# Kernel tuning notes

Hardware: AMD Instinct MI355X
Metric: run time of the kernel (lower is better)

Reference implementation:

```python
import jax, jax.numpy as jnp
import numpy as np

D_MODEL = 2048
D_STATE = 64
D_CONV = 4
EXPAND = 2
HEADDIM = 64
NGROUPS = 1
CHUNK = 64
D_INNER = EXPAND * D_MODEL            # 4096
NHEADS = D_INNER // HEADDIM           # 64
D_XBC = D_INNER + 2 * NGROUPS * D_STATE
D_IN_PROJ = 2 * D_INNER + 2 * NGROUPS * D_STATE + NHEADS


def setup_inputs():
    key = jax.random.key(0)
    ks = jax.random.split(key, 8)
    B, L = 2, 4096
    u = jax.random.normal(ks[0], (B, L, D_MODEL), jnp.float32)
    W_in = jax.random.normal(ks[1], (D_IN_PROJ, D_MODEL), jnp.float32) * 0.02
    conv_w = jax.random.normal(ks[2], (D_XBC, D_CONV), jnp.float32) * 0.2
    conv_b = jnp.zeros((D_XBC,), jnp.float32)
    dt = jnp.exp(jax.random.uniform(ks[3], (NHEADS,)) * (np.log(0.1) - np.log(0.001)) + np.log(0.001))
    dt = jnp.clip(dt, 1e-4)
    dt_bias = dt + jnp.log(-jnp.expm1(-dt))
    A_log = jnp.log(jax.random.uniform(ks[4], (NHEADS,), minval=1.0, maxval=16.0))
    D_param = jnp.ones((NHEADS,), jnp.float32)
    norm_w = jnp.ones((D_INNER,), jnp.float32)
    W_out = jax.random.normal(ks[5], (D_MODEL, D_INNER), jnp.float32) * 0.02
    return dict(u=u, W_in=W_in, conv_w=conv_w, conv_b=conv_b, dt_bias=dt_bias,
                A_log=A_log, D_param=D_param, norm_w=norm_w, W_out=W_out)


def segsum(x):
    # x: (..., T) -> (..., T, T) with entry [l,s] = sum_{s< i <= l} x[i], -inf above diag
    T = x.shape[-1]
    mask_strict = jnp.tril(jnp.ones((T, T), bool), k=-1)
    mask_incl = jnp.tril(jnp.ones((T, T), bool), k=0)
    xe = jnp.where(mask_strict, x[..., :, None], 0.0)  # element [l,s] = x[l] if l>s
    xseg = jnp.cumsum(xe, axis=-2)
    return jnp.where(mask_incl, xseg, -jnp.inf)


def ssd_scan(X, A, Bm, Cm, block_len=CHUNK):
    # X: (b,L,h,p), A: (b,L,h), Bm/Cm: (b,L,h,n)
    b, seqlen, h, p = X.shape
    n = Bm.shape[-1]
    pad_len = (block_len - seqlen % block_len) % block_len
    if pad_len > 0:
        X = jnp.pad(X, ((0, 0), (0, pad_len), (0, 0), (0, 0)))
        A = jnp.pad(A, ((0, 0), (0, pad_len), (0, 0)))
        Bm = jnp.pad(Bm, ((0, 0), (0, pad_len), (0, 0), (0, 0)))
        Cm = jnp.pad(Cm, ((0, 0), (0, pad_len), (0, 0), (0, 0)))
    L = X.shape[1]
    c = L // block_len
    Xc = X.reshape(b, c, block_len, h, p)
    Ac = A.reshape(b, c, block_len, h).transpose(0, 3, 1, 2)  # (b,h,c,l)
    Bc = Bm.reshape(b, c, block_len, h, n)
    Cc = Cm.reshape(b, c, block_len, h, n)
    A_cum = jnp.cumsum(Ac, axis=-1)                           # (b,h,c,l)
    Lmat = jnp.exp(segsum(Ac))                                # (b,h,c,l,s)
    CB = jnp.einsum('bclhn,bcshn->bhcls', Cc, Bc)
    Y_diag = jnp.einsum('bhcls,bcshp->bhclp', CB * Lmat, Xc)
    decay_states = jnp.exp(A_cum[..., -1:] - A_cum)           # (b,h,c,l)
    states = jnp.einsum('bhcl,bclhn,bclhp->bhcpn', decay_states, Bc, Xc)
    init = jnp.zeros((b, h, 1, p, n), X.dtype)
    states = jnp.concatenate([init, states], axis=2)          # (b,h,c+1,p,n)
    chunk_decay = jnp.pad(A_cum[..., -1], ((0, 0), (0, 0), (1, 0)))  # (b,h,c+1)
    decay_chunk = jnp.exp(segsum(chunk_decay))                # (b,h,c+1,c+1)
    new_states = jnp.einsum('bhzc,bhcpn->bhzpn', decay_chunk, states)[:, :, :-1]
    Y_off = jnp.einsum('bclhn,bhcpn,bhcl->bhclp', Cc, new_states, jnp.exp(A_cum))
    Y = (Y_diag + Y_off).transpose(0, 2, 3, 1, 4).reshape(b, L, h, p)
    if pad_len > 0:
        Y = Y[:, :seqlen]
    return Y


def rmsnorm_grouped(x, w, ngroups, eps=1e-5):
    gs = x.shape[-1] // ngroups
    xg = x.reshape(*x.shape[:-1], ngroups, gs)
    xg = xg * jax.lax.rsqrt(jnp.mean(xg * xg, axis=-1, keepdims=True) + eps)
    return xg.reshape(x.shape) * w


def reference(u, W_in, conv_w, conv_b, dt_bias, A_log, D_param, norm_w, W_out):
    B, L, _ = u.shape
    zxbcdt = u @ W_in.T                                      # (B,L,d_in_proj)
    z = zxbcdt[..., :D_INNER]
    xBC = zxbcdt[..., D_INNER:D_INNER + D_XBC]
    dt = zxbcdt[..., D_INNER + D_XBC:]
    # causal depthwise conv1d, kernel D_CONV, left-pad D_CONV-1
    xpad = jnp.pad(xBC, ((0, 0), (D_CONV - 1, 0), (0, 0)))
    conv = conv_b
    for k in range(D_CONV):
        conv = conv + conv_w[:, k] * xpad[:, k:k + L, :]
    xBC = jax.nn.silu(conv)
    x = xBC[..., :D_INNER].reshape(B, L, NHEADS, HEADDIM)
    B_ssm = xBC[..., D_INNER:D_INNER + NGROUPS * D_STATE].reshape(B, L, NGROUPS, D_STATE)
    C_ssm = xBC[..., D_INNER + NGROUPS * D_STATE:].reshape(B, L, NGROUPS, D_STATE)
    if NGROUPS < NHEADS:
        rep = NHEADS // NGROUPS
        B_ssm = jnp.repeat(B_ssm, rep, axis=2)
        C_ssm = jnp.repeat(C_ssm, rep, axis=2)
    dt = jax.nn.softplus(dt + dt_bias)                        # (B,L,nheads)
    A = -jnp.exp(A_log)                                       # (nheads,)
    y = ssd_scan(x * dt[..., None], A * dt, B_ssm, C_ssm, block_len=CHUNK)
    y = y + D_param[:, None] * x
    y = y.reshape(B, L, D_INNER)
    y = rmsnorm_grouped(y * jax.nn.silu(z), norm_w, NGROUPS)
    return y @ W_out.T
```

## Files before the change

### kernel.cpp

```cpp
#include <hip/hip_runtime.h>
#include <hip/hip_bf16.h>
#include <math.h>

#define SEQ       4096
#define DMODEL    2048
#define DINNER    4096
#define DXBC      4224
#define NPROJ     8384
#define NHEADS    64
#define HDIM      64
#define DSTATE    64
#define NCHUNK    64
#define XLD       4352

typedef __attribute__((ext_vector_type(8))) _Float16 half8;
typedef __attribute__((ext_vector_type(2))) _Float16 half2v;
typedef __attribute__((ext_vector_type(4))) float floatx4;

__device__ __forceinline__ void async_copy16(void* lds, const void* g) {
  __builtin_amdgcn_global_load_lds(
      (const __attribute__((address_space(1))) unsigned int*)g,
      (__attribute__((address_space(3))) unsigned int*)lds, 16, 0, 0);
}

__device__ __forceinline__ float silu_f(float x) { return x / (1.f + __expf(-x)); }

__device__ __forceinline__ void cvt8(const float* __restrict__ s, _Float16* __restrict__ d) {
  float4 a = *(const float4*)s;
  float4 b = *(const float4*)(s + 4);
  half8 h;
  h[0] = (_Float16)a.x; h[1] = (_Float16)a.y; h[2] = (_Float16)a.z; h[3] = (_Float16)a.w;
  h[4] = (_Float16)b.x; h[5] = (_Float16)b.y; h[6] = (_Float16)b.z; h[7] = (_Float16)b.w;
  *(half8*)d = h;
}

__global__ void diag_kernel(float* out, float v) { out[0] = v; }

__global__ void cvt8_kernel(const float* __restrict__ src, _Float16* __restrict__ dst, int n8) {
  int i = blockIdx.x * 256 + threadIdx.x;
  if (i < n8) cvt8(src + (size_t)i * 8, dst + (size_t)i * 8);
}

#define U_N8 (SEQ * DMODEL / 8)
__global__ void cvt_in_kernel(const float* __restrict__ u, const float* __restrict__ W_in,
                              _Float16* __restrict__ ubf, _Float16* __restrict__ winbf) {
  int i = blockIdx.x * 256 + threadIdx.x;
  if (i < U_N8) {
    cvt8(u + (size_t)i * 8, ubf + (size_t)i * 8);
  } else {
    int j = i - U_N8;
    int row = j >> 8;
    size_t off = (size_t)j * 8;
    if (row < NPROJ) {
      cvt8(W_in + off, winbf + off);
    } else {
      half8 zz = {};
      *(half8*)(winbf + off) = zz;
    }
  }
}

template <typename OT>
__global__ __launch_bounds__(256) void gemm_bt64(
    const _Float16* __restrict__ A, const _Float16* __restrict__ B,
    OT* __restrict__ C0, OT* __restrict__ C1, int K,
    int ldc0, int ldc1, int ncol0, int tiles_m, int tiles_n) {
  __shared__ __align__(16) _Float16 As[128 * 64];
  __shared__ __align__(16) _Float16 Bs[128 * 64];
  int t = threadIdx.x;
  int nt = tiles_m * tiles_n;
  int id = blockIdx.x;
  int id2 = ((nt & 7) == 0) ? ((id & 7) * (nt >> 3) + (id >> 3)) : id;
  int wband = tiles_m << 2;
  int g = id2 / wband;
  int rm = id2 - g * wband;
  int bw = tiles_n - (g << 2); if (bw > 4) bw = 4;
  int pn = (g << 2) + rm % bw;
  int pm = rm / bw;
  int m0 = pm * 128, n0 = pn * 128;

  int w = t >> 6, lane = t & 63, q = lane >> 4, r = lane & 15;
  int wm = (w >> 1) * 64, wn = (w & 1) * 64;
  int rowoff = lane >> 3;
  int chunkoff = ((lane & 7) ^ rowoff) * 8;
  const _Float16* gA[4];
  const _Float16* gB[4];
#pragma unroll
  for (int i = 0; i < 4; ++i) {
    gA[i] = A + (size_t)(m0 + i * 32 + w * 8 + rowoff) * K + chunkoff;
    gB[i] = B + (size_t)(n0 + i * 32 + w * 8 + rowoff) * K + chunkoff;
  }
  floatx4 acc[4][4] = {};
  for (int k0 = 0; k0 < K; k0 += 64) {
#pragma unroll
    for (int i = 0; i < 4; ++i) {
      async_copy16(As + (i * 32 + w * 8) * 64, gA[i] + k0);
      async_copy16(Bs + (i * 32 + w * 8) * 64, gB[i] + k0);
    }
    __syncthreads();
#pragma unroll
    for (int kk = 0; kk < 64; kk += 32) {
      half8 af[4], bf[4];
#pragma unroll
      for (int im = 0; im < 4; ++im) {
        int R = wm + im * 16 + r;
        af[im] = *(const half8*)&As[R * 64 + ((((kk >> 3) + q) ^ (R & 7)) << 3)];
      }
#pragma unroll
      for (int in = 0; in < 4; ++in) {
        int R = wn + in * 16 + r;
        bf[in] = *(const half8*)&Bs[R * 64 + ((((kk >> 3) + q) ^ (R & 7)) << 3)];
      }
#pragma unroll
      for (int im = 0; im < 4; ++im)
#pragma unroll
        for (int in = 0; in < 4; ++in)
          acc[im][in] =
              __builtin_amdgcn_mfma_f32_16x16x32_f16(af[im], bf[in], acc[im][in], 0, 0, 0);
    }
    __syncthreads();
  }
  OT* Cp = (n0 < ncol0) ? C0 : C1;
  int ldc = (n0 < ncol0) ? ldc0 : ldc1;
  int cb = (n0 < ncol0) ? n0 : n0 - ncol0;
#pragma unroll
  for (int im = 0; im < 4; ++im)
#pragma unroll
    for (int in = 0; in < 4; ++in)
#pragma unroll
      for (int i = 0; i < 4; ++i)
        Cp[(size_t)(m0 + wm + im * 16 + q * 4 + i) * ldc + cb + wn + in * 16 + r] =
            (OT)acc[im][in][i];
}

template <typename OT>
__global__ __launch_bounds__(512, 2) void gemm256(
    const _Float16* __restrict__ A, const _Float16* __restrict__ B,
    OT* __restrict__ C0, OT* __restrict__ C1, int K,
    int ldc0, int ldc1, int ncol0, int tiles_m, int tiles_n) {
  __shared__ __align__(16) _Float16 As[2][256 * 64];
  __shared__ __align__(16) _Float16 Bs[2][256 * 64];
  int t = threadIdx.x;
  int nwg = tiles_m * tiles_n;
  int id = blockIdx.x;
  int wgid = ((nwg & 7) == 0) ? ((id & 7) * (nwg >> 3) + (id >> 3)) : id;
  int wband = tiles_m << 2;
  int g = wgid / wband;
  int rm = wgid - g * wband;
  int bw = tiles_n - (g << 2); if (bw > 4) bw = 4;
  int pn = (g << 2) + rm % bw;
  int pm = rm / bw;
  int m0 = pm * 256, n0 = pn * 256;

  int w = t >> 6, lane = t & 63, q4 = lane >> 4, r16 = lane & 15;
  int srow = lane >> 3;
  int schunk = ((lane & 7) ^ srow) << 3;
  const _Float16* gAb = A + (size_t)(m0 + w * 8 + srow) * K + schunk;
  const _Float16* gBb = B + (size_t)(n0 + w * 8 + srow) * K + schunk;
  int Ra = (w >> 2) * 128 + r16;
  int Rb = (w & 3) * 64 + r16;

  unsigned aLds = (unsigned)(unsigned long long)
      (const __attribute__((address_space(3))) void*)(const void*)&As[0][0];
  unsigned bLds = (unsigned)(unsigned long long)
      (const __attribute__((address_space(3))) void*)(const void*)&Bs[0][0];
  int x0 = (q4 ^ (r16 & 7)) << 4;
  int x1 = ((4 + q4) ^ (r16 & 7)) << 4;
  unsigned baseA00 = aLds + Ra * 128 + x0;
  unsigned baseA01 = aLds + Ra * 128 + x1;
  unsigned baseA10 = baseA00 + 32768;
  unsigned baseA11 = baseA01 + 32768;
  unsigned baseB00 = bLds + Rb * 128 + x0;
  unsigned baseB01 = bLds + Rb * 128 + x1;
  unsigned baseB10 = baseB00 + 32768;
  unsigned baseB11 = baseB01 + 32768;

  floatx4 acc[8][4] = {};
  half8 afA[4], afB[4];
  half8 bfA[4], bfB[4];

#define DSR__(dst, base, off)                                                  \
  asm volatile("ds_read_b128 %0, %1 offset:" #off : "=v"(dst) : "v"(base))
#define DSR(dst, base, off) DSR__(dst, base, off)
#define LDA_LO(afX, bA) { DSR(afX[0], bA, 0);    DSR(afX[1], bA, 2048);        \
                          DSR(afX[2], bA, 4096); DSR(afX[3], bA, 6144); }
#define LDA_HI(afX, bA) { DSR(afX[0], bA, 8192);  DSR(afX[1], bA, 10240);      \
                          DSR(afX[2], bA, 12288); DSR(afX[3], bA, 14336); }
#define LDB4(bfX, bB)   { DSR(bfX[0], bB, 0);    DSR(bfX[1], bB, 2048);        \
                          DSR(bfX[2], bB, 4096); DSR(bfX[3], bB, 6144); }
#define STAGE(buf_, kt_)                                                       \
  {                                                                            \
    _Pragma("unroll") for (int i_ = 0; i_ < 4; ++i_)                           \
        async_copy16(&As[buf_][(i_ * 64 + w * 8) * 64],                        \
                     gAb + (size_t)(i_ * 64) * K + ((kt_) << 6));              \
    _Pragma("unroll") for (int i_ = 0; i_ < 4; ++i_)                           \
        async_copy16(&Bs[buf_][(i_ * 64 + w * 8) * 64],                        \
                     gBb + (size_t)(i_ * 64) * K + ((kt_) << 6));              \
  }
#define MMP(afX, bfX, mh_)                                                     \
  __builtin_amdgcn_s_setprio(1);                                               \
  _Pragma("unroll") for (int mi_ = 0; mi_ < 4; ++mi_)                          \
  _Pragma("unroll") for (int ni_ = 0; ni_ < 4; ++ni_)                          \
      acc[(mh_)*4 + mi_][ni_] = __builtin_amdgcn_mfma_f32_16x16x32_f16(        \
          afX[mi_], bfX[ni_], acc[(mh_)*4 + mi_][ni_], 0, 0, 0);               \
  __builtin_amdgcn_s_setprio(0);
#define BARF() { __builtin_amdgcn_s_barrier(); asm volatile("" ::: "memory"); }
#define WLG(n)                                                                 \
  {                                                                            \
    asm volatile("s_waitcnt lgkmcnt(" #n ")" ::: "memory");                    \
    __builtin_amdgcn_sched_barrier(0);                                         \
  }
#define TILE(ktv, bA0, bA1, bB1, CURB, bA0n, bB0n)                             \
  {                                                                            \
    LDA_HI(afB, bA0);                                                          \
    WLG(4); MMP(afA, bfA, 0);                                                  \
    LDA_LO(afA, bA1); LDB4(bfB, bB1);                                          \
    WLG(8); MMP(afB, bfA, 1);                                                  \
    LDA_HI(afB, bA1);                                                          \
    WLG(4); MMP(afA, bfB, 0);                                                  \
    WLG(0);                                                                    \
    BARF();                                                                    \
    if ((ktv) + 2 < NT) {                                                      \
      STAGE(CURB, (ktv) + 2);                                                  \
      asm volatile("s_waitcnt vmcnt(8)" ::: "memory");                         \
    } else {                                                                   \
      asm volatile("s_waitcnt vmcnt(0)" ::: "memory");                         \
    }                                                                          \
    BARF();                                                                    \
    if ((ktv) + 1 < NT) { LDA_LO(afA, bA0n); LDB4(bfA, bB0n); }                \
    __builtin_amdgcn_sched_barrier(0);                                         \
    MMP(afB, bfB, 1);                                                          \
  }

  int NT = K >> 6;
  STAGE(0, 0);
  STAGE(1, 1);
  asm volatile("s_waitcnt vmcnt(8)" ::: "memory");
  BARF();
  LDA_LO(afA, baseA00);
  LDB4(bfA, baseB00);

  for (int kt = 0; kt < NT; kt += 2) {
    TILE(kt,     baseA00, baseA01, baseB01, 0, baseA10, baseB10);
    TILE(kt + 1, baseA10, baseA11, baseB11, 1, baseA00, baseB00);
  }

#pragma unroll
  for (int mi = 0; mi < 8; ++mi) {
    int rb = m0 + (w >> 2) * 128 + mi * 16 + q4 * 4;
    OT* Cp = (n0 < ncol0) ? C0 : C1;
    int ldc = (n0 < ncol0) ? ldc0 : ldc1;
    int cb0 = ((n0 < ncol0) ? n0 : n0 - ncol0) + (w & 3) * 64 + r16;
#pragma unroll
    for (int ni = 0; ni < 4; ++ni)
#pragma unroll
      for (int i = 0; i < 4; ++i)
        Cp[(size_t)(rb + i) * ldc + cb0 + ni * 16] = (OT)acc[mi][ni][i];
  }
#undef DSR__
#undef DSR
#undef LDA_LO
#undef LDA_HI
#undef LDB4
#undef STAGE
#undef MMP
#undef BARF
#undef WLG
#undef TILE
}

#define CONVB (SEQ * (DXBC / 2) / 256)
__global__ __launch_bounds__(256) void conv_dtscan_kernel(
    const _Float16* __restrict__ xin, const float* __restrict__ conv_w,
    const float* __restrict__ conv_b, _Float16* __restrict__ xcv,
    const float* __restrict__ dt_bias, const float* __restrict__ A_log,
    float* __restrict__ dtp, float* __restrict__ acum, float* __restrict__ chs) {
  int t = threadIdx.x;
  if (blockIdx.x < CONVB) {
    int idx = blockIdx.x * 256 + t;
    int l = idx / (DXBC / 2);
    int c = (idx - l * (DXBC / 2)) * 2;
    const _Float16* zc = xin + (size_t)l * XLD + c;
    float a0 = conv_b[c], a1 = conv_b[c + 1];
#pragma unroll
    for (int k = 0; k < 4; ++k) {
      int off = k - 3;
      if (l + off >= 0) {
        half2v v = *(const half2v*)(zc + (long)off * XLD);
        a0 += conv_w[c * 4 + k] * (float)v[0];
        a1 += conv_w[c * 4 + 4 + k] * (float)v[1];
      }
    }
    half2v o;
    o[0] = (_Float16)silu_f(a0);
    o[1] = (_Float16)silu_f(a1);
    *(half2v*)(xcv + (size_t)l * DXBC + c) = o;
  } else {
    __shared__ float dAs[64 * 65];
    int c = blockIdx.x - CONVB;
    int h = t & 63;
    const _Float16* dtraw = xin + DXBC;
    float bias = dt_bias[h];
    float negA = -__expf(A_log[h]);
#pragma unroll
    for (int i = 0; i < 16; ++i) {
      int l = i * 4 + (t >> 6);
      int row = c * 64 + l;
      float x = (float)dtraw[(size_t)row * XLD + h] + bias;
      float dtv = (x > 20.f) ? x : log1pf(__expf(x));
      dtp[(size_t)row * 64 + h] = dtv;
      dAs[l * 65 + h] = negA * dtv;
    }
    __syncthreads();
    if (t < 64) {
      float a = 0.f;
      size_t base = ((size_t)c * 64 + t) * 64;
      for (int l = 0; l < 64; ++l) {
        a += dAs[l * 65 + t];
        acum[base + l] = a;
      }
      chs[c * 64 + t] = a;
    }
  }
}

__global__ __launch_bounds__(256) void states_kernel(
    const _Float16* __restrict__ xcv, const float* __restrict__ dtp,
    const float* __restrict__ acum, const float* __restrict__ chs,
    _Float16* __restrict__ states) {
  int bid = blockIdx.x;
  int c = bid & 63, h = bid >> 6;
  int row0 = c * 64;
  int acbase = (c * 64 + h) * 64;
  __shared__ __align__(16) _Float16 XdT[64 * 72];
  __shared__ __align__(16) _Float16 BdT[64 * 72];
  __shared__ float dec[64];
  int t = threadIdx.x;
  if (t < 64) dec[t] = __expf(chs[acbase >> 6] - acum[acbase + t]);
  __syncthreads();
#pragma unroll
  for (int i = 0; i < 16; ++i) {
    int flat = i * 256 + t;
    int l = flat >> 6, col = flat & 63;
    int grow = row0 + l;
    float dtv = dtp[(size_t)grow * 64 + h];
    float xv = (float)xcv[(size_t)grow * DXBC + h * 64 + col] * dtv;
    XdT[col * 72 + l] = (_Float16)xv;
    float bv = (float)xcv[(size_t)grow * DXBC + DINNER + col] * dec[l];
    BdT[col * 72 + l] = (_Float16)bv;
  }
  __syncthreads();
  int w = t >> 6, lane = t & 63, q = lane >> 4, r = lane & 15;
#pragma unroll
  for (int in = 0; in < 4; ++in) {
    floatx4 a4 = {0.f, 0.f, 0.f, 0.f};
#pragma unroll
    for (int k0 = 0; k0 < 64; k0 += 32) {
      half8 af = *(const half8*)&XdT[(w * 16 + r) * 72 + k0 + q * 8];
      half8 bf = *(const half8*)&BdT[(in * 16 + r) * 72 + k0 + q * 8];
      a4 = __builtin_amdgcn_mfma_f32_16x16x32_f16(af, bf, a4, 0, 0, 0);
    }
#pragma unroll
    for (int i = 0; i < 4; ++i)
      states[((size_t)bid * 64 + (w * 16 + q * 4 + i)) * 64 + in * 16 + r] = (_Float16)a4[i];
  }
}

__global__ __launch_bounds__(256) void scan_kernel(_Float16* __restrict__ states,
                                                   const float* __restrict__ chs) {
  int bid = blockIdx.x;
  int h = bid >> 4, seg = bid & 15;
  size_t base = ((size_t)h * 64) * 4096 + seg * 256 + threadIdx.x;
  float carry = 0.f;
  float s_cur = (float)states[base];
  for (int c = 0; c < 64; ++c) {
    size_t idx = base + (size_t)c * 4096;
    float s_next = (c < 63) ? (float)states[idx + 4096] : 0.f;
    float ec = __expf(chs[c * 64 + h]);
    states[idx] = (_Float16)carry;
    carry = carry * ec + s_cur;
    s_cur = s_next;
  }
}

__global__ __launch_bounds__(256) void yout_kernel(
    const _Float16* __restrict__ xcv, const float* __restrict__ dtp,
    const float* __restrict__ acum, const _Float16* __restrict__ sin_,
    const float* __restrict__ Dp, _Float16* __restrict__ Y) {
  int bid = blockIdx.x;
  int c = bid & 63, h = bid >> 6;
  int row0 = c * 64;
  int acbase = (c * 64 + h) * 64;
  __shared__ __align__(16) _Float16 Cs[64 * 72];
  __shared__ __align__(16) _Float16 Bt[64 * 72];
  __shared__ __align__(16) _Float16 XdT[64 * 72];
  __shared__ __align__(16) _Float16 Ms[64 * 72];
  __shared__ float acs[64];
  int t = threadIdx.x;
  if (t < 64) acs[t] = acum[acbase + t];
#pragma unroll
  for (int i = 0; i < 16; ++i) {
    int flat = i * 256 + t;
    int l = flat >> 6, col = flat & 63;
    int grow = row0 + l;
    const _Float16* rp = xcv + (size_t)grow * DXBC;
    Cs[l * 72 + col] = rp[DINNER + DSTATE + col];
    Bt[l * 72 + col] = rp[DINNER + col];
    float xv = (float)rp[h * 64 + col] * dtp[(size_t)grow * 64 + h];
    XdT[col * 72 + l] = (_Float16)xv;
  }
  __syncthreads();
  int w = t >> 6, lane = t & 63, q = lane >> 4, r = lane & 15;
  int m = w * 16 + r;
#pragma unroll
  for (int in = 0; in < 4; ++in) {
    floatx4 cb = {0.f, 0.f, 0.f, 0.f};
#pragma unroll
    for (int k0 = 0; k0 < 64; k0 += 32) {
      half8 af = *(const half8*)&Cs[m * 72 + k0 + q * 8];
      half8 bf = *(const half8*)&Bt[(in * 16 + r) * 72 + k0 + q * 8];
      cb = __builtin_amdgcn_mfma_f32_16x16x32_f16(af, bf, cb, 0, 0, 0);
    }
#pragma unroll
    for (int i = 0; i < 4; ++i) {
      int l = w * 16 + q * 4 + i;
      int s = in * 16 + r;
      float v = (s <= l) ? cb[i] * __expf(acs[l] - acs[s]) : 0.f;
      Ms[l * 72 + s] = (_Float16)v;
    }
  }
  __syncthreads();
  size_t sbase = (size_t)bid * 4096;
  float Dh = Dp[h];
#pragma unroll
  for (int in = 0; in < 4; ++in) {
    floatx4 acc = {0.f, 0.f, 0.f, 0.f};
#pragma unroll
    for (int k0 = 0; k0 < 64; k0 += 32) {
      half8 af = *(const half8*)&Cs[m * 72 + k0 + q * 8];
      half8 bf = *(const half8*)&sin_[sbase + (size_t)(in * 16 + r) * 64 + k0 + q * 8];
      acc = __builtin_amdgcn_mfma_f32_16x16x32_f16(af, bf, acc, 0, 0, 0);
    }
#pragma unroll
    for (int i = 0; i < 4; ++i) acc[i] *= __expf(acs[w * 16 + q * 4 + i]);
#pragma unroll
    for (int k0 = 0; k0 < 64; k0 += 32) {
      half8 af = *(const half8*)&Ms[m * 72 + k0 + q * 8];
      half8 bf = *(const half8*)&XdT[(in * 16 + r) * 72 + k0 + q * 8];
      acc = __builtin_amdgcn_mfma_f32_16x16x32_f16(af, bf, acc, 0, 0, 0);
    }
#pragma unroll
    for (int i = 0; i < 4; ++i) {
      int l = w * 16 + q * 4 + i;
      int p = in * 16 + r;
      int grow = row0 + l;
      float xv = (float)xcv[(size_t)grow * DXBC + h * 64 + p];
      Y[(size_t)grow * DINNER + h * 64 + p] = (_Float16)(acc[i] + Dh * xv);
    }
  }
}

__global__ __launch_bounds__(256) void rmsnorm_kernel(const _Float16* __restrict__ Y,
                                                      _Float16* __restrict__ Z,
                                                      const float* __restrict__ norm_w) {
  int row = blockIdx.x;
  const half8* y8 = (const half8*)(Y + (size_t)row * DINNER);
  half8* z8 = (half8*)(Z + (size_t)row * DINNER);
  __shared__ float red[4];
  int t = threadIdx.x;
  float g[16];
  float ss = 0.f;
#pragma unroll
  for (int i = 0; i < 2; ++i) {
    int j = i * 256 + t;
    half8 yv = y8[j];
    half8 zv = z8[j];
#pragma unroll
    for (int e = 0; e < 8; ++e) {
      float gv = (float)yv[e] * silu_f((float)zv[e]);
      g[i * 8 + e] = gv;
      ss += gv * gv;
    }
  }
#pragma unroll
  for (int o = 32; o > 0; o >>= 1) ss += __shfl_down(ss, o, 64);
  if ((t & 63) == 0) red[t >> 6] = ss;
  __syncthreads();
  float rs = rsqrtf((red[0] + red[1] + red[2] + red[3]) / (float)DINNER + 1e-5f);
#pragma unroll
  for (int i = 0; i < 2; ++i) {
    int j = i * 256 + t;
    const float4* w4 = (const float4*)(norm_w + j * 8);
    float4 wa = w4[0], wb = w4[1];
    half8 o;
    o[0] = (_Float16)(g[i * 8 + 0] * rs * wa.x);
    o[1] = (_Float16)(g[i * 8 + 1] * rs * wa.y);
    o[2] = (_Float16)(g[i * 8 + 2] * rs * wa.z);
    o[3] = (_Float16)(g[i * 8 + 3] * rs * wa.w);
    o[4] = (_Float16)(g[i * 8 + 4] * rs * wb.x);
    o[5] = (_Float16)(g[i * 8 + 5] * rs * wb.y);
    o[6] = (_Float16)(g[i * 8 + 6] * rs * wb.z);
    o[7] = (_Float16)(g[i * 8 + 7] * rs * wb.w);
    z8[j] = o;
  }
}

extern "C" void kernel_launch(void* const* d_in, const int* in_sizes, int n_in,
                              void* d_out, int out_size, void* d_ws, size_t ws_size,
                              hipStream_t stream) {
  const float* u       = (const float*)d_in[0];
  const float* W_in    = (const float*)d_in[1];
  const float* conv_w  = (const float*)d_in[2];
  const float* conv_b  = (const float*)d_in[3];
  const float* dt_bias = (const float*)d_in[4];
  const float* A_log   = (const float*)d_in[5];
  const float* D_param = (const float*)d_in[6];
  const float* norm_w  = (const float*)d_in[7];
  const float* W_out   = (const float*)d_in[8];
  float* out = (float*)d_out;
  char* ws = (char*)d_ws;

  const size_t NEED_MID   = 192954368ULL;
  const size_t NEED_SMALL = 140525568ULL;
  bool big = (ws_size >= NEED_MID);
  if (!big && ws_size < NEED_SMALL) {
    diag_kernel<<<1, 1, 0, stream>>>(out, (float)ws_size);
    return;
  }

  if (big) {
    _Float16* zb     = (_Float16*)(ws + 0);
    _Float16* xbcdtb = (_Float16*)(ws + 67108864ULL);
    _Float16* xcv    = (_Float16*)(ws + 102760448ULL);
    _Float16* winbf  = xcv;
    _Float16* states = (_Float16*)(ws + 137363456ULL);
    _Float16* ubf    = states;
    _Float16* woutbf = (_Float16*)(ws + 170917888ULL);
    float* dtp  = (float*)(ws + 187695104ULL);
    float* acum = (float*)(ws + 188743680ULL);
    float* chs  = (float*)(ws + 189792256ULL);

    cvt8_kernel<<<DMODEL * DINNER / 8 / 256, 256, 0, stream>>>(
        W_out, woutbf, DMODEL * DINNER / 8);

    for (int b = 0; b < 2; ++b) {
      const float* ub = u + (size_t)b * SEQ * DMODEL;
      _Float16* zbb = zb + (size_t)b * SEQ * DINNER;

      cvt_in_kernel<<<U_N8 / 256 + 8448, 256, 0, stream>>>(ub, W_in, ubf, winbf);

      gemm256<_Float16><<<512, 512, 0, stream>>>(
          ubf, winbf, zbb, xbcdtb, DMODEL, DINNER, XLD, DINNER, 16, 32);
      gemm_bt64<_Float16><<<64, 256, 0, stream>>>(
          ubf, winbf + (size_t)2 * DINNER * DMODEL, xbcdtb + DINNER, xbcdtb + DINNER,
          DMODEL, XLD, XLD, 1 << 30, 32, 2);

      conv_dtscan_kernel<<<CONVB + NCHUNK, 256, 0, stream>>>(
          xbcdtb, conv_w, conv_b, xcv, dt_bias, A_log, dtp, acum, chs);

      states_kernel<<<NHEADS * NCHUNK, 256, 0, stream>>>(xcv, dtp, acum, chs, states);
      scan_kernel<<<NHEADS * 16, 256, 0, stream>>>(states, chs);
      yout_kernel<<<NHEADS * NCHUNK, 256, 0, stream>>>(xcv, dtp, acum, states, D_param,
                                                       xbcdtb );

      rmsnorm_kernel<<<SEQ, 256, 0, stream>>>(xbcdtb, zbb, norm_w);
    }

    gemm256<float><<<256, 512, 0, stream>>>(
        zb, woutbf, out, out, DINNER, DMODEL, DMODEL, 1 << 30, 32, 8);
  } else {
    _Float16* zb     = (_Float16*)(ws + 0);
    _Float16* xbcdtb = (_Float16*)(ws + 33554432ULL);
    _Float16* Yb     = xbcdtb;
    _Float16* xcv    = (_Float16*)(ws + 69206016ULL);
    _Float16* winbf  = xcv;
    _Float16* states = (_Float16*)(ws + 103809024ULL);
    _Float16* ubf    = states;
    _Float16* woutbf = states;
    float* dtp  = (float*)(ws + 137363456ULL);
    float* acum = (float*)(ws + 139460608ULL);
    float* chs  = (float*)(ws + 140509184ULL);

    for (int b = 0; b < 2; ++b) {
      const float* ub = u + (size_t)b * SEQ * DMODEL;
      float* outb = out + (size_t)b * SEQ * DMODEL;

      cvt_in_kernel<<<U_N8 / 256 + 8448, 256, 0, stream>>>(ub, W_in, ubf, winbf);
      gemm_bt64<_Float16><<<32 * 66, 256, 0, stream>>>(
          ubf, winbf, zb, xbcdtb, DMODEL, DINNER, XLD, DINNER, 32, 66);
      conv_dtscan_kernel<<<CONVB + NCHUNK, 256, 0, stream>>>(
          xbcdtb, conv_w, conv_b, xcv, dt_bias, A_log, dtp, acum, chs);
      states_kernel<<<NHEADS * NCHUNK, 256, 0, stream>>>(xcv, dtp, acum, chs, states);
      scan_kernel<<<NHEADS * 16, 256, 0, stream>>>(states, chs);
      yout_kernel<<<NHEADS * NCHUNK, 256, 0, stream>>>(xcv, dtp, acum, states, D_param, Yb);
      rmsnorm_kernel<<<SEQ, 256, 0, stream>>>(Yb, zb, norm_w);
      cvt8_kernel<<<DMODEL * DINNER / 8 / 256, 256, 0, stream>>>(
          W_out, woutbf, DMODEL * DINNER / 8);
      gemm_bt64<float><<<32 * 16, 256, 0, stream>>>(
          zb, woutbf, outb, outb, DINNER, DMODEL, DMODEL, 1 << 30, 32, 16);
    }
  }
}
```

Baseline: 1.116 ms.

## Restructure GEMM mainloop into quadrant-staged pipeline with half-tile async loads

Reorganizes the 256x256 fp16 MFMA GEMM main loop. The per-wave output is now split into four 64x64-style quadrants computed in sequence, and global-to-LDS loads for the next K tile are issued in A/B half-tile pieces between quadrant computations. This replaces the previous two-tile-ahead double buffer with fine-grained lgkm waits. The aim is a finer interleave of memory traffic and compute with reuse of A/B fragments across quadrants. In exchange it adds many more barriers and full lgkmcnt(0) waits, which may serialize LDS reads against MFMA. Prefetch depth also drops to one tile ahead.

```diff
diff --git a/kernel.cpp b/kernel.cpp
--- a/kernel.cpp
+++ b/kernel.cpp
@@ -157,8 +157,6 @@
   int schunk = ((lane & 7) ^ srow) << 3;
   const _Float16* gAb = A + (size_t)(m0 + w * 8 + srow) * K + schunk;
   const _Float16* gBb = B + (size_t)(n0 + w * 8 + srow) * K + schunk;
-  int Ra = (w >> 2) * 128 + r16;
-  int Rb = (w & 3) * 64 + r16;
 
   unsigned aLds = (unsigned)(unsigned long long)
       (const __attribute__((address_space(3))) void*)(const void*)&As[0][0];
@@ -166,106 +164,123 @@
       (const __attribute__((address_space(3))) void*)(const void*)&Bs[0][0];
   int x0 = (q4 ^ (r16 & 7)) << 4;
   int x1 = ((4 + q4) ^ (r16 & 7)) << 4;
-  unsigned baseA00 = aLds + Ra * 128 + x0;
-  unsigned baseA01 = aLds + Ra * 128 + x1;
-  unsigned baseA10 = baseA00 + 32768;
-  unsigned baseA11 = baseA01 + 32768;
-  unsigned baseB00 = bLds + Rb * 128 + x0;
-  unsigned baseB01 = bLds + Rb * 128 + x1;
-  unsigned baseB10 = baseB00 + 32768;
-  unsigned baseB11 = baseB01 + 32768;
-
-  floatx4 acc[8][4] = {};
-  half8 afA[4], afB[4];
-  half8 bfA[4], bfB[4];
-
-#define DSR__(dst, base, off)                                                  \
+  unsigned bA00 = aLds + (w >> 2) * 8192 + r16 * 128 + x0;
+  unsigned bA01 = aLds + (w >> 2) * 8192 + r16 * 128 + x1;
+  unsigned bA10 = bA00 + 32768, bA11 = bA01 + 32768;
+  unsigned bB00 = bLds + (w & 3) * 4096 + r16 * 128 + x0;
+  unsigned bB01 = bLds + (w & 3) * 4096 + r16 * 128 + x1;
+  unsigned bB10 = bB00 + 32768, bB11 = bB01 + 32768;
+
+  floatx4 acc[4][4][2] = {};
+  half8 af[4][2];
+  half8 bfL[2][2], bfH[2][2];
+
+#define DSR(dst, base, off)                                                    \
   asm volatile("ds_read_b128 %0, %1 offset:" #off : "=v"(dst) : "v"(base))
-#define DSR(dst, base, off) DSR__(dst, base, off)
-#define LDA_LO(afX, bA) { DSR(afX[0], bA, 0);    DSR(afX[1], bA, 2048);        \
-                          DSR(afX[2], bA, 4096); DSR(afX[3], bA, 6144); }
-#define LDA_HI(afX, bA) { DSR(afX[0], bA, 8192);  DSR(afX[1], bA, 10240);      \
-                          DSR(afX[2], bA, 12288); DSR(afX[3], bA, 14336); }
-#define LDB4(bfX, bB)   { DSR(bfX[0], bB, 0);    DSR(bfX[1], bB, 2048);        \
-                          DSR(bfX[2], bB, 4096); DSR(bfX[3], bB, 6144); }
-#define STAGE(buf_, kt_)                                                       \
-  {                                                                            \
-    _Pragma("unroll") for (int i_ = 0; i_ < 4; ++i_)                           \
-        async_copy16(&As[buf_][(i_ * 64 + w * 8) * 64],                        \
-                     gAb + (size_t)(i_ * 64) * K + ((kt_) << 6));              \
-    _Pragma("unroll") for (int i_ = 0; i_ < 4; ++i_)                           \
-        async_copy16(&Bs[buf_][(i_ * 64 + w * 8) * 64],                        \
-                     gBb + (size_t)(i_ * 64) * K + ((kt_) << 6));              \
-  }
-#define MMP(afX, bfX, mh_)                                                     \
+#define LDA_LOH(b0, b1) { DSR(af[0][0], b0, 0);     DSR(af[0][1], b1, 0);      \
+                          DSR(af[1][0], b0, 2048);  DSR(af[1][1], b1, 2048);   \
+                          DSR(af[2][0], b0, 4096);  DSR(af[2][1], b1, 4096);   \
+                          DSR(af[3][0], b0, 6144);  DSR(af[3][1], b1, 6144); }
+#define LDA_HIH(b0, b1) { DSR(af[0][0], b0, 16384); DSR(af[0][1], b1, 16384);  \
+                          DSR(af[1][0], b0, 18432); DSR(af[1][1], b1, 18432);  \
+                          DSR(af[2][0], b0, 20480); DSR(af[2][1], b1, 20480);  \
+                          DSR(af[3][0], b0, 22528); DSR(af[3][1], b1, 22528); }
+#define LDB_LOH(bf, b0, b1) { DSR(bf[0][0], b0, 0);     DSR(bf[0][1], b1, 0);  \
+                              DSR(bf[1][0], b0, 2048);  DSR(bf[1][1], b1, 2048); }
+#define LDB_HIH(bf, b0, b1) { DSR(bf[0][0], b0, 16384); DSR(bf[0][1], b1, 16384); \
+                              DSR(bf[1][0], b0, 18432); DSR(bf[1][1], b1, 18432); }
+#define STAGE_A(buf_, H_, kt_)                                                 \
+  { _Pragma("unroll") for (int i_ = 0; i_ < 2; ++i_)                           \
+        async_copy16(&As[buf_][((H_)*128 + i_ * 64 + w * 8) * 64],             \
+                     gAb + (size_t)((H_)*128 + i_ * 64) * K + ((kt_) << 6)); }
+#define STAGE_B(buf_, H_, kt_)                                                 \
+  { _Pragma("unroll") for (int i_ = 0; i_ < 2; ++i_)                           \
+        async_copy16(&Bs[buf_][((H_)*128 + i_ * 64 + w * 8) * 64],             \
+                     gBb + (size_t)((H_)*128 + i_ * 64) * K + ((kt_) << 6)); }
+#define MM(qd, bf)                                                             \
   __builtin_amdgcn_s_setprio(1);                                               \
   _Pragma("unroll") for (int mi_ = 0; mi_ < 4; ++mi_)                          \
-  _Pragma("unroll") for (int ni_ = 0; ni_ < 4; ++ni_)                          \
-      acc[(mh_)*4 + mi_][ni_] = __builtin_amdgcn_mfma_f32_16x16x32_f16(        \
-          afX[mi_], bfX[ni_], acc[(mh_)*4 + mi_][ni_], 0, 0, 0);               \
+  _Pragma("unroll") for (int ni_ = 0; ni_ < 2; ++ni_)                          \
+  _Pragma("unroll") for (int k_ = 0; k_ < 2; ++k_)                             \
+      acc[qd][mi_][ni_] = __builtin_amdgcn_mfma_f32_16x16x32_f16(              \
+          af[mi_][k_], bf[ni_][k_], acc[qd][mi_][ni_], 0, 0, 0);               \
   __builtin_amdgcn_s_setprio(0);
 #define BARF() { __builtin_amdgcn_s_barrier(); asm volatile("" ::: "memory"); }
-#define WLG(n)                                                                 \
+#define LGKM0()                                                                \
+  { asm volatile("s_waitcnt lgkmcnt(0)" ::: "memory");                         \
+    __builtin_amdgcn_sched_barrier(0); }
+#define VM(n) asm volatile("s_waitcnt vmcnt(" #n ")" ::: "memory")
+
+#define TILE(ktv, aK0, aK1, bK0, bK1, NXTB)                                    \
   {                                                                            \
-    asm volatile("s_waitcnt lgkmcnt(" #n ")" ::: "memory");                    \
+                                         \
+    LDA_LOH(aK0, aK1);                                                         \
+    LDB_LOH(bfL, bK0, bK1);                                                    \
+    if ((ktv) + 1 < NT) { STAGE_A(NXTB, 0, (ktv) + 1); VM(4); } else VM(2);    \
+    BARF(); LGKM0();                                                           \
+    MM(0, bfL);                                                                \
+    BARF();                                                                    \
+                              \
+    LDB_HIH(bfH, bK0, bK1);                                                    \
+    if ((ktv) + 1 < NT) { STAGE_B(NXTB, 0, (ktv) + 1); VM(4); } else VM(0);    \
+    BARF(); LGKM0();                                                           \
+    MM(1, bfH);                                                                \
+    BARF();                                                                    \
+                             \
+    LDA_HIH(aK0, aK1);                                                         \
+    if ((ktv) + 1 < NT) STAGE_B(NXTB, 1, (ktv) + 1);                           \
+    BARF(); LGKM0();                                                           \
+    MM(2, bfH);                                                                \
+    BARF();                                                                    \
+                        \
+    if ((ktv) + 1 < NT) { STAGE_A(NXTB, 1, (ktv) + 1); VM(4); }                \
+    BARF();                                                                    \
     __builtin_amdgcn_sched_barrier(0);                                         \
-  }
-#define TILE(ktv, bA0, bA1, bB1, CURB, bA0n, bB0n)                             \
-  {                                                                            \
-    LDA_HI(afB, bA0);                                                          \
-    WLG(4); MMP(afA, bfA, 0);                                                  \
-    LDA_LO(afA, bA1); LDB4(bfB, bB1);                                          \
-    WLG(8); MMP(afB, bfA, 1);                                                  \
-    LDA_HI(afB, bA1);                                                          \
-    WLG(4); MMP(afA, bfB, 0);                                                  \
-    WLG(0);                                                                    \
+    MM(3, bfL);                                                                \
     BARF();                                                                    \
-    if ((ktv) + 2 < NT) {                                                      \
-      STAGE(CURB, (ktv) + 2);                                                  \
-      asm volatile("s_waitcnt vmcnt(8)" ::: "memory");                         \
-    } else {                                                                   \
-      asm volatile("s_waitcnt vmcnt(0)" ::: "memory");                         \
-    }                                                                          \
-    BARF();                                                                    \
-    if ((ktv) + 1 < NT) { LDA_LO(afA, bA0n); LDB4(bfA, bB0n); }                \
-    __builtin_amdgcn_sched_barrier(0);                                         \
-    MMP(afB, bfB, 1);                                                          \
   }
 
   int NT = K >> 6;
-  STAGE(0, 0);
-  STAGE(1, 1);
-  asm volatile("s_waitcnt vmcnt(8)" ::: "memory");
+  STAGE_A(0, 0, 0);
+  STAGE_B(0, 0, 0);
+  STAGE_B(0, 1, 0);
+  STAGE_A(0, 1, 0);
+  VM(4);
   BARF();
-  LDA_LO(afA, baseA00);
-  LDB4(bfA, baseB00);
 
   for (int kt = 0; kt < NT; kt += 2) {
-    TILE(kt,     baseA00, baseA01, baseB01, 0, baseA10, baseB10);
-    TILE(kt + 1, baseA10, baseA11, baseB11, 1, baseA00, baseB00);
-  }
-
-#pragma unroll
-  for (int mi = 0; mi < 8; ++mi) {
-    int rb = m0 + (w >> 2) * 128 + mi * 16 + q4 * 4;
-    OT* Cp = (n0 < ncol0) ? C0 : C1;
-    int ldc = (n0 < ncol0) ? ldc0 : ldc1;
-    int cb0 = ((n0 < ncol0) ? n0 : n0 - ncol0) + (w & 3) * 64 + r16;
-#pragma unroll
-    for (int ni = 0; ni < 4; ++ni)
-#pragma unroll
-      for (int i = 0; i < 4; ++i)
-        Cp[(size_t)(rb + i) * ldc + cb0 + ni * 16] = (OT)acc[mi][ni][i];
-  }
-#undef DSR__
+    TILE(kt,     bA00, bA01, bB00, bB01, 1);
+    TILE(kt + 1, bA10, bA11, bB10, bB11, 0);
+  }
+
+  const int paC[4] = {0, 0, 1, 1};
+  const int pbC[4] = {0, 1, 1, 0};
+  OT* Cp = (n0 < ncol0) ? C0 : C1;
+  int ldc = (n0 < ncol0) ? ldc0 : ldc1;
+  int cbase = (n0 < ncol0) ? n0 : n0 - ncol0;
+#pragma unroll
+  for (int qd = 0; qd < 4; ++qd) {
+    int rb = m0 + paC[qd] * 128 + (w >> 2) * 64 + q4 * 4;
+    int cb = cbase + pbC[qd] * 128 + (w & 3) * 32 + r16;
+#pragma unroll
+    for (int mi = 0; mi < 4; ++mi)
+#pragma unroll
+      for (int ni = 0; ni < 2; ++ni)
+#pragma unroll
+        for (int i = 0; i < 4; ++i)
+          Cp[(size_t)(rb + mi * 16 + i) * ldc + cb + ni * 16] = (OT)acc[qd][mi][ni][i];
+  }
 #undef DSR
-#undef LDA_LO
-#undef LDA_HI
-#undef LDB4
-#undef STAGE
-#undef MMP
+#undef LDA_LOH
+#undef LDA_HIH
+#undef LDB_LOH
+#undef LDB_HIH
+#undef STAGE_A
+#undef STAGE_B
+#undef MM
 #undef BARF
-#undef WLG
+#undef LGKM0
+#undef VM
 #undef TILE
 }
 
```

New measurement: 1.065 ms. 4.6% less time.
